# Kernel optimization log

Hardware: AMD Instinct MI355X
Metric: run time of the kernel (lower is better)

The kernel has to match this reference:

```python
import jax, jax.numpy as jnp
import numpy as np
import math

B = 8; SEQ = 1000; C_IN = 32; D = 512; H = 8; DK = 64; DV = 64
DFF = 2048; NL = 4; ARY = 4; INNER = 5


def get_mask_np(seq_size, ary, inner):
    # full k-ary tree sizes (padded) and effective sizes per scale
    full = 1
    while full < seq_size:
        full *= ary
    all_size = [full]; effe = [seq_size]
    while all_size[-1] > 1:
        all_size.append(all_size[-1] // ary)
        effe.append(math.ceil(effe[-1] / ary))
    n = sum(all_size)
    allow = np.zeros((n, n), dtype=bool)
    w = inner // 2
    starts = np.concatenate([[0], np.cumsum(all_size)]).astype(int)
    # intra-scale local window
    for l, sz in enumerate(all_size):
        s = starts[l]
        for i in range(sz):
            lo = max(i - w, 0); hi = min(i + w + 1, sz)
            allow[s + i, s + lo:s + hi] = True
    # inter-scale parent<->children links
    for l in range(1, len(all_size)):
        s = starts[l]; ps = starts[l - 1]
        for i in range(all_size[l]):
            lo = ps + i * ary; hi = ps + (i + 1) * ary
            allow[s + i, lo:hi] = True
            allow[lo:hi, s + i] = True
    return allow, all_size, effe

ALLOW_NP, ALL_SIZE, EFFE_SIZE = get_mask_np(SEQ, ARY, INNER)
NTOT = sum(ALL_SIZE)   # 1365
DEPTH = len(ALL_SIZE)  # 6
OFFS = np.concatenate([[0], np.cumsum(ALL_SIZE)]).astype(int)


def sinusoid_pe(length, d):
    pos = np.arange(length)[:, None].astype(np.float64)
    i = np.arange(d)[None, :]
    ang = pos / np.power(10000.0, (2 * (i // 2)) / d)
    pe = np.zeros((length, d), np.float32)
    pe[:, 0::2] = np.sin(ang[:, 0::2]); pe[:, 1::2] = np.cos(ang[:, 1::2])
    return pe

PE_NP = sinusoid_pe(SEQ, D)


def layer_norm(x, s, b, eps=1e-5):
    m = x.mean(-1, keepdims=True)
    v = ((x - m) ** 2).mean(-1, keepdims=True)
    return (x - m) * jax.lax.rsqrt(v + eps) * s + b


def setup_inputs() -> dict:
    key = jax.random.key(0)
    ks = jax.random.split(key, 10)
    p = lambda k, shape, sc=0.02: jax.random.normal(k, shape, jnp.float32) * sc
    return {
        "x": jax.random.normal(ks[0], (B, SEQ, C_IN), jnp.float32),
        "conv_w": p(ks[1], (D, C_IN, 3), 0.05),
        "norm_s": jnp.ones((D,), jnp.float32), "norm_b": jnp.zeros((D,), jnp.float32),
        "wq": p(ks[2], (NL, D, H * DK)), "wk": p(ks[3], (NL, D, H * DK)),
        "wv": p(ks[4], (NL, D, H * DV)), "wo": p(ks[5], (NL, H * DV, D)),
        "ln1_s": jnp.ones((NL, D), jnp.float32), "ln1_b": jnp.zeros((NL, D), jnp.float32),
        "w1": p(ks[6], (NL, D, DFF)), "b1": jnp.zeros((NL, DFF), jnp.float32),
        "w2": p(ks[7], (NL, DFF, D)), "b2": jnp.zeros((NL, D), jnp.float32),
        "ln2_s": jnp.ones((NL, D), jnp.float32), "ln2_b": jnp.zeros((NL, D), jnp.float32),
    }


def reference(x, conv_w, norm_s, norm_b, wq, wk, wv, wo, ln1_s, ln1_b,
              w1, b1, w2, b2, ln2_s, ln2_b):
    allow = jnp.asarray(ALLOW_NP)        # [N,N] True = attend
    pe = jnp.asarray(PE_NP)              # [S,D]
    # --- DataEmbedding: conv1d(k=3, circular pad, no bias) + sinusoid PE ---
    xt = jnp.concatenate([x[:, -1:], x, x[:, :1]], axis=1)       # (B,S+2,C)
    emb = jax.lax.conv_general_dilated(
        xt, conv_w, (1,), 'VALID', dimension_numbers=('NWC', 'OIW', 'NWC'))
    emb = emb + pe[None]                                          # (B,S,D)
    # pad sequence to full-tree leaf count
    emb = jnp.pad(emb, ((0, 0), (0, ALL_SIZE[0] - SEQ), (0, 0)))  # (B,L0,D)
    # --- MaxPooling_Construct: pool by ary per level, concat, LayerNorm ---
    parts = [emb]
    cur = emb
    for lvl in range(DEPTH - 1):
        L = cur.shape[1]
        cur = cur.reshape(B, L // ARY, ARY, D).max(axis=2)
        parts.append(cur)
    seq = jnp.concatenate(parts, axis=1)                          # (B,N,D)
    seq = layer_norm(seq, norm_s, norm_b)
    # --- masked MHA encoder layers (post-norm) ---
    scale = 1.0 / math.sqrt(DK)
    neg = jnp.float32(-1e9)
    for l in range(NL):
        q = (seq @ wq[l]).reshape(B, NTOT, H, DK)
        k = (seq @ wk[l]).reshape(B, NTOT, H, DK)
        v = (seq @ wv[l]).reshape(B, NTOT, H, DV)
        scores = jnp.einsum('bnhd,bmhd->bhnm', q, k) * scale
        scores = jnp.where(allow[None, None], scores, neg)
        attn = jax.nn.softmax(scores, axis=-1)
        ctx = jnp.einsum('bhnm,bmhd->bnhd', attn, v).reshape(B, NTOT, H * DV)
        seq = layer_norm(seq + ctx @ wo[l], ln1_s[l], ln1_b[l])
        ff = jax.nn.gelu(seq @ w1[l] + b1[l], approximate=False) @ w2[l] + b2[l]
        seq = layer_norm(seq + ff, ln2_s[l], ln2_b[l])
    # --- keep only the effective (unpadded) prefix of each scale ---
    out = jnp.concatenate(
        [seq[:, OFFS[i]:OFFS[i] + EFFE_SIZE[i]] for i in range(DEPTH)], axis=1)
    return out  # (B, sum(effe)=1334, D)
```

## Files before the change

kernel.cpp:

```cpp
#include <hip/hip_runtime.h>
#include <cstdint>
#include <math.h>

#define DEV __device__ __forceinline__

static constexpr int BQ = 8, SEQN = 1000, CIN = 32, NH = 8;
static constexpr int NLAY = 4;
static constexpr int NTOT_C = 1365;
static constexpr int M_REAL = BQ * NTOT_C;
static constexpr int M_PAD  = 11008;

DEV float bf2f(unsigned short u){ return __uint_as_float(((unsigned)u) << 16); }
DEV unsigned short f2bf(float f){
  unsigned u = __float_as_uint(f);
  u += 0x7fffu + ((u >> 16) & 1u);
  return (unsigned short)(u >> 16);
}

typedef __bf16 bf16x8 __attribute__((ext_vector_type(8)));
typedef float  f32x4  __attribute__((ext_vector_type(4)));
typedef unsigned short u16x8 __attribute__((ext_vector_type(8)));

#define GLD_LDS16(gp, lp) __builtin_amdgcn_global_load_lds( \
    (const __attribute__((address_space(1))) void*)(gp), \
    (__attribute__((address_space(3))) void*)(lp), 16, 0, 0)

template<int N> DEV void waitcnt_vm(){
  asm volatile("s_waitcnt vmcnt(%0)" :: "i"(N) : "memory");
}
DEV void waitcnt_lgkm0(){ asm volatile("s_waitcnt lgkmcnt(0)" ::: "memory"); }
DEV void cfence(){ asm volatile("" ::: "memory"); }

DEV float gelu_f(float x){
  float z = 0.7978845608028654f * (x + 0.044715f * x * x * x);
  z = fminf(fmaxf(z, -10.f), 10.f);
  float e = __expf(2.f * z);
  float th = (e - 1.f) / (e + 1.f);
  return 0.5f * x * (1.f + th);
}

__global__ __launch_bounds__(256) void pe_kernel(float* __restrict__ pe)
{
  int idx = blockIdx.x * 256 + threadIdx.x;
  int d = idx & 511, s = idx >> 9;
  if (s >= SEQN) return;
  float e2 = (float)(d & ~1);
  float freq = exp2f(e2 * (-13.287712379549449f / 512.0f));
  float ang = (float)s * freq;
  pe[idx] = (d & 1) ? cosf(ang) : sinf(ang);
}

__global__ __launch_bounds__(256) void conv_kernel(const float* __restrict__ x,
    const float* __restrict__ w, const float* __restrict__ pe, float* __restrict__ seqf)
{
  __shared__ float ws_w[128 * 97];
  __shared__ __align__(16) float xs[66][32];
  int b = blockIdx.z, s0 = blockIdx.y * 64, d0 = blockIdx.x * 128;
  int tid = threadIdx.x;
  for (int i = tid; i < 128 * 96; i += 256){
    int r = i / 96, c = i - r * 96;
    ws_w[r * 97 + c] = w[(size_t)(d0 + r) * 96 + c];
  }
  for (int i = tid; i < 66 * 32; i += 256){
    int r = i >> 5, c = i & 31;
    int ss = s0 + r - 1;
    ss = (ss < 0) ? (ss + SEQN) : (ss >= SEQN ? ss - SEQN : ss);
    xs[r][c] = x[((size_t)b * SEQN + ss) * CIN + c];
  }
  __syncthreads();
  int dl = tid & 127, sh = tid >> 7;
  float wr[96];
  #pragma unroll
  for (int i = 0; i < 96; i++) wr[i] = ws_w[dl * 97 + i];
  int d = d0 + dl;
  for (int si = 0; si < 32; si++){
    int sl = sh * 32 + si;
    int s = s0 + sl;
    float acc = 0.f;
    #pragma unroll
    for (int kk = 0; kk < 3; kk++){
      const float* xr = xs[sl + kk];
      #pragma unroll
      for (int c = 0; c < 32; c++) acc += xr[c] * wr[c * 3 + kk];
    }
    float outv = (s < SEQN) ? acc + pe[(size_t)s * 512 + d] : 0.f;
    seqf[((size_t)b * NTOT_C + s) * 512 + d] = outv;
  }
}

__global__ __launch_bounds__(256) void pool_kernel(float* __restrict__ seqf,
    int inOff, int outOff, int outSz)
{
  int e = blockIdx.x * 256 + threadIdx.x;
  int d = e & 511;
  int r = e >> 9;
  int i = r % outSz;
  int b = r / outSz;
  const float* src = seqf + ((size_t)b * NTOT_C + inOff + 4 * i) * 512 + d;
  float m = fmaxf(fmaxf(src[0], src[512]), fmaxf(src[1024], src[1536]));
  seqf[((size_t)b * NTOT_C + outOff + i) * 512 + d] = m;
}

__global__ __launch_bounds__(256) void ln4_kernel(const float* __restrict__ xin,
    float* __restrict__ outf, unsigned short* __restrict__ outb,
    const float* __restrict__ sg, const float* __restrict__ bg, int M)
{
  int row = blockIdx.x * 4 + (threadIdx.x >> 6);
  int lane = threadIdx.x & 63;
  size_t base = (size_t)row * 512 + lane * 8;
  if (row >= M){
    f32x4 z4 = {0.f, 0.f, 0.f, 0.f};
    *reinterpret_cast<f32x4*>(outf + base) = z4;
    *reinterpret_cast<f32x4*>(outf + base + 4) = z4;
    u16x8 z8 = {0, 0, 0, 0, 0, 0, 0, 0};
    *reinterpret_cast<u16x8*>(outb + base) = z8;
    return;
  }
  f32x4 v0 = *reinterpret_cast<const f32x4*>(xin + base);
  f32x4 v1 = *reinterpret_cast<const f32x4*>(xin + base + 4);
  float sall = v0[0] + v0[1] + v0[2] + v0[3] + v1[0] + v1[1] + v1[2] + v1[3];
  #pragma unroll
  for (int o = 32; o; o >>= 1) sall += __shfl_xor(sall, o, 64);
  float mean = sall * (1.f / 512.f);
  float d[8];
  #pragma unroll
  for (int e = 0; e < 4; e++){ d[e] = v0[e] - mean; d[4 + e] = v1[e] - mean; }
  float sq = 0.f;
  #pragma unroll
  for (int e = 0; e < 8; e++) sq += d[e] * d[e];
  #pragma unroll
  for (int o = 32; o; o >>= 1) sq += __shfl_xor(sq, o, 64);
  float rstd = 1.f / sqrtf(sq * (1.f / 512.f) + 1e-5f);
  f32x4 s0 = *reinterpret_cast<const f32x4*>(sg + lane * 8);
  f32x4 s1 = *reinterpret_cast<const f32x4*>(sg + lane * 8 + 4);
  f32x4 g0 = *reinterpret_cast<const f32x4*>(bg + lane * 8);
  f32x4 g1 = *reinterpret_cast<const f32x4*>(bg + lane * 8 + 4);
  f32x4 y0, y1; u16x8 yb;
  #pragma unroll
  for (int e = 0; e < 4; e++){
    y0[e] = d[e] * rstd * s0[e] + g0[e];
    y1[e] = d[4 + e] * rstd * s1[e] + g1[e];
    yb[e] = f2bf(y0[e]); yb[4 + e] = f2bf(y1[e]);
  }
  *reinterpret_cast<f32x4*>(outf + base) = y0;
  *reinterpret_cast<f32x4*>(outf + base + 4) = y1;
  *reinterpret_cast<u16x8*>(outb + base) = yb;
}

template<bool WRITEF>
__global__ __launch_bounds__(256) void lnres4_kernel(const unsigned short* __restrict__ cin,
    float* __restrict__ outf, unsigned short* __restrict__ seqb,
    const float* __restrict__ sg, const float* __restrict__ bg, int M)
{
  int row = blockIdx.x * 4 + (threadIdx.x >> 6);
  int lane = threadIdx.x & 63;
  size_t base = (size_t)row * 512 + lane * 8;
  if (row >= M){
    u16x8 z8 = {0, 0, 0, 0, 0, 0, 0, 0};
    *reinterpret_cast<u16x8*>(seqb + base) = z8;
    if (WRITEF){
      f32x4 z4 = {0.f, 0.f, 0.f, 0.f};
      *reinterpret_cast<f32x4*>(outf + base) = z4;
      *reinterpret_cast<f32x4*>(outf + base + 4) = z4;
    }
    return;
  }
  u16x8 cv = *reinterpret_cast<const u16x8*>(cin + base);
  u16x8 rv = *reinterpret_cast<const u16x8*>(seqb + base);
  float v[8];
  #pragma unroll
  for (int e = 0; e < 8; e++) v[e] = bf2f(cv[e]) + bf2f(rv[e]);
  float sall = 0.f;
  #pragma unroll
  for (int e = 0; e < 8; e++) sall += v[e];
  #pragma unroll
  for (int o = 32; o; o >>= 1) sall += __shfl_xor(sall, o, 64);
  float mean = sall * (1.f / 512.f);
  float sq = 0.f;
  #pragma unroll
  for (int e = 0; e < 8; e++){ v[e] -= mean; sq += v[e] * v[e]; }
  #pragma unroll
  for (int o = 32; o; o >>= 1) sq += __shfl_xor(sq, o, 64);
  float rstd = 1.f / sqrtf(sq * (1.f / 512.f) + 1e-5f);
  f32x4 s0 = *reinterpret_cast<const f32x4*>(sg + lane * 8);
  f32x4 s1 = *reinterpret_cast<const f32x4*>(sg + lane * 8 + 4);
  f32x4 g0 = *reinterpret_cast<const f32x4*>(bg + lane * 8);
  f32x4 g1 = *reinterpret_cast<const f32x4*>(bg + lane * 8 + 4);
  u16x8 yb; f32x4 y0, y1;
  #pragma unroll
  for (int e = 0; e < 4; e++){
    y0[e] = v[e] * rstd * s0[e] + g0[e];
    y1[e] = v[4 + e] * rstd * s1[e] + g1[e];
    yb[e] = f2bf(y0[e]); yb[4 + e] = f2bf(y1[e]);
  }
  *reinterpret_cast<u16x8*>(seqb + base) = yb;
  if (WRITEF){
    *reinterpret_cast<f32x4*>(outf + base) = y0;
    *reinterpret_cast<f32x4*>(outf + base + 4) = y1;
  }
}

__global__ __launch_bounds__(256) void wconv_all(
    const float* __restrict__ wq, const float* __restrict__ wk,
    const float* __restrict__ wv, const float* __restrict__ wo,
    const float* __restrict__ w1, const float* __restrict__ w2,
    unsigned short* __restrict__ qkvT, unsigned short* __restrict__ woT,
    unsigned short* __restrict__ w1T, unsigned short* __restrict__ w2T)
{
  __shared__ float tile[32][33];
  int bid = blockIdx.x;
  const float* wl; unsigned short* wtl; int N, K, n0, k0;
  if (bid < 4096){
    int part = bid >> 10, t = bid & 1023;
    int l = t >> 8, t2 = t & 255;
    k0 = (t2 >> 4) * 32; n0 = (t2 & 15) * 32;
    N = 512; K = 512;
    const float* s = (part == 0) ? wq : (part == 1) ? wk : (part == 2) ? wv : wo;
    wl = s + (size_t)l * 512 * 512;
    wtl = (part < 3) ? (qkvT + (size_t)l * 1536 * 512 + (size_t)part * 512 * 512)
                     : (woT + (size_t)l * 512 * 512);
  } else if (bid < 8192){
    int t = bid - 4096, l = t >> 10, t2 = t & 1023;
    k0 = (t2 >> 6) * 32; n0 = (t2 & 63) * 32;
    N = 2048; K = 512;
    wl = w1 + (size_t)l * 512 * 2048;
    wtl = w1T + (size_t)l * 2048 * 512;
  } else {
    int t = bid - 8192, l = t >> 10, t2 = t & 1023;
    k0 = (t2 >> 4) * 32; n0 = (t2 & 15) * 32;
    N = 512; K = 2048;
    wl = w2 + (size_t)l * 2048 * 512;
    wtl = w2T + (size_t)l * 512 * 2048;
  }
  int c = threadIdx.x & 31, r8 = threadIdx.x >> 5;
  #pragma unroll
  for (int p = 0; p < 4; p++){ int r = r8 + p * 8; tile[r][c] = wl[(size_t)(k0 + r) * N + n0 + c]; }
  __syncthreads();
  #pragma unroll
  for (int p = 0; p < 4; p++){ int r = r8 + p * 8; wtl[(size_t)(n0 + r) * K + k0 + c] = f2bf(tile[c][r]); }
}

template<int EPI, int BM, int BN>
__global__ __launch_bounds__(256) void gemm2_kernel(
    const unsigned short* __restrict__ A, const unsigned short* __restrict__ Wt,
    unsigned short* __restrict__ Cb, const float* __restrict__ bias, int N, int K)
{
  constexpr int MF = BM / 32, NF = BN / 32;
  constexpr int LA = BM / 32, LB = BN / 32;
  __shared__ __align__(16) unsigned short Abuf[2][BM * 64];
  __shared__ __align__(16) unsigned short Bbuf[2][BN * 64];
  const int tid = threadIdx.x;
  const int wid = tid >> 6, lane = tid & 63;
  const int wm2 = wid >> 1, wn2 = wid & 1;
  const int r16 = lane & 15, g = lane >> 4;
  const int m0 = blockIdx.y * BM, n0 = blockIdx.x * BN;

  const int row0 = tid >> 3;
  const int scol = ((tid & 7) ^ (row0 & 7)) * 8;
  const unsigned short* gAs = A  + (size_t)(m0 + row0) * K + scol;
  const unsigned short* gBs = Wt + (size_t)(n0 + row0) * K + scol;

  const int swz0 = ((0 + g) ^ (r16 & 7)) * 8;
  const int swz1 = ((4 + g) ^ (r16 & 7)) * 8;
  const int arow = (wm2 * (BM / 2) + r16) * 64;
  const int brow = (wn2 * (BN / 2) + r16) * 64;

  const int nt = K >> 6;
  f32x4 acc[MF][NF] = {};

  auto STAGE_A = [&](int buf, int kt){
    #pragma unroll
    for (int q = 0; q < LA; q++)
      GLD_LDS16(gAs + kt * 64 + (size_t)q * 32 * K, &Abuf[buf][q * 2048 + tid * 8]);
  };
  auto STAGE_B = [&](int buf, int kt){
    #pragma unroll
    for (int q = 0; q < LB; q++)
      GLD_LDS16(gBs + kt * 64 + (size_t)q * 32 * K, &Bbuf[buf][q * 2048 + tid * 8]);
  };

  cfence();
  STAGE_A(0, 0); STAGE_B(0, 0);
  if (nt > 1){ STAGE_A(1, 1); waitcnt_vm<LA>(); }
  else        { waitcnt_vm<0>(); }
  __builtin_amdgcn_s_barrier();
  cfence();

  for (int t = 0; t < nt; t++){
    const int d = t & 1;
    const unsigned short* Ab = Abuf[d];
    const unsigned short* Bb = Bbuf[d];

    bf16x8 a0[MF], b0[NF];
    #pragma unroll
    for (int m = 0; m < MF; m++) a0[m] = *reinterpret_cast<const bf16x8*>(&Ab[arow + m * 1024 + swz0]);
    #pragma unroll
    for (int n = 0; n < NF; n++) b0[n] = *reinterpret_cast<const bf16x8*>(&Bb[brow + n * 1024 + swz0]);
    if (t + 1 < nt){ cfence(); STAGE_B(d ^ 1, t + 1); cfence(); }
    __builtin_amdgcn_s_setprio(1);
    #pragma unroll
    for (int m = 0; m < MF; m++)
      #pragma unroll
      for (int n = 0; n < NF; n++)
        acc[m][n] = __builtin_amdgcn_mfma_f32_16x16x32_bf16(a0[m], b0[n], acc[m][n], 0, 0, 0);
    __builtin_amdgcn_s_setprio(0);

    bf16x8 a1[MF], b1v[NF];
    #pragma unroll
    for (int m = 0; m < MF; m++) a1[m] = *reinterpret_cast<const bf16x8*>(&Ab[arow + m * 1024 + swz1]);
    #pragma unroll
    for (int n = 0; n < NF; n++) b1v[n] = *reinterpret_cast<const bf16x8*>(&Bb[brow + n * 1024 + swz1]);
    waitcnt_lgkm0();
    __builtin_amdgcn_s_barrier();
    cfence();
    if (t + 2 < nt){ STAGE_A(d, t + 2); cfence(); }
    __builtin_amdgcn_s_setprio(1);
    #pragma unroll
    for (int m = 0; m < MF; m++)
      #pragma unroll
      for (int n = 0; n < NF; n++)
        acc[m][n] = __builtin_amdgcn_mfma_f32_16x16x32_bf16(a1[m], b1v[n], acc[m][n], 0, 0, 0);
    __builtin_amdgcn_s_setprio(0);

    if (t + 1 < nt){
      if (t + 2 < nt) waitcnt_vm<LA>();
      else            waitcnt_vm<0>();
      __builtin_amdgcn_s_barrier();
      cfence();
    }
  }

  const int colBase = n0 + wn2 * (BN / 2) + r16;
  #pragma unroll
  for (int m = 0; m < MF; m++){
    int row = m0 + wm2 * (BM / 2) + m * 16 + g * 4;
    #pragma unroll
    for (int n = 0; n < NF; n++){
      int col = colBase + n * 16;
      float bsv = (EPI >= 2) ? bias[col] : 0.f;
      #pragma unroll
      for (int j = 0; j < 4; j++){
        float v = acc[m][n][j];
        if (EPI >= 2) v += bsv;
        if (EPI == 2) v = gelu_f(v);
        Cb[(size_t)(row + j) * N + col] = f2bf(v);
      }
    }
  }
}

__global__ __launch_bounds__(256) void attn_kernel(
    const unsigned short* __restrict__ qkv, unsigned short* __restrict__ ctx)
{
  int wid = blockIdx.x * 4 + (threadIdx.x >> 6);
  int lane = threadIdx.x & 63;
  int n = wid % NTOT_C;
  int b = wid / NTOT_C;

  int i, sz, of, cb, par;
  if (n < 1024){ i = n;        sz = 1024; of = 0;    cb = -1;            par = 1024 + (i >> 2); }
  else if (n < 1280){ i = n - 1024; sz = 256; of = 1024; cb = 0    + 4 * i; par = 1280 + (i >> 2); }
  else if (n < 1344){ i = n - 1280; sz = 64;  of = 1280; cb = 1024 + 4 * i; par = 1344 + (i >> 2); }
  else if (n < 1360){ i = n - 1344; sz = 16;  of = 1344; cb = 1280 + 4 * i; par = 1360 + (i >> 2); }
  else if (n < 1364){ i = n - 1360; sz = 4;   of = 1360; cb = 1344 + 4 * i; par = 1364; }
  else { i = 0; sz = 1; of = 1364; cb = 1360; par = -1; }

  int nb[10];
  #pragma unroll
  for (int s5 = 0; s5 < 5; s5++){ int pos = i - 2 + s5; nb[s5] = (pos >= 0 && pos < sz) ? of + pos : -1; }
  #pragma unroll
  for (int r = 0; r < 4; r++) nb[5 + r] = (cb >= 0) ? cb + r : -1;
  nb[9] = par;

  const unsigned short* rows = qkv + ((size_t)b * NTOT_C) * 1536;

  u16x8 qv = *reinterpret_cast<const u16x8*>(rows + (size_t)n * 1536 + lane * 8);
  float qf[8];
  #pragma unroll
  for (int e = 0; e < 8; e++) qf[e] = bf2f(qv[e]);

  float sc[10];
  #pragma unroll
  for (int j = 0; j < 10; j++){
    int id = nb[j] >= 0 ? nb[j] : n;
    u16x8 kv = *reinterpret_cast<const u16x8*>(rows + (size_t)id * 1536 + 512 + lane * 8);
    float p = 0.f;
    #pragma unroll
    for (int e = 0; e < 8; e++) p += qf[e] * bf2f(kv[e]);
    p += __shfl_xor(p, 1, 64);
    p += __shfl_xor(p, 2, 64);
    p += __shfl_xor(p, 4, 64);
    sc[j] = (nb[j] >= 0) ? p * 0.125f : -1e30f;
  }
  float mx = sc[0];
  #pragma unroll
  for (int j = 1; j < 10; j++) mx = fmaxf(mx, sc[j]);
  float den = 0.f;
  float wj[10];
  #pragma unroll
  for (int j = 0; j < 10; j++){
    wj[j] = (nb[j] >= 0) ? expf(sc[j] - mx) : 0.f;
    den += wj[j];
  }
  float rden = 1.f / den;
  float accv[8] = {};
  #pragma unroll
  for (int j = 0; j < 10; j++){
    int id = nb[j] >= 0 ? nb[j] : n;
    u16x8 vv = *reinterpret_cast<const u16x8*>(rows + (size_t)id * 1536 + 1024 + lane * 8);
    float w = wj[j];
    #pragma unroll
    for (int e = 0; e < 8; e++) accv[e] += w * bf2f(vv[e]);
  }
  u16x8 ov;
  #pragma unroll
  for (int e = 0; e < 8; e++) ov[e] = f2bf(accv[e] * rden);
  *reinterpret_cast<u16x8*>(ctx + ((size_t)b * NTOT_C + n) * 512 + lane * 8) = ov;
}

__global__ __launch_bounds__(256) void gather_kernel(const float* __restrict__ seqf,
    float* __restrict__ out)
{
  int e = blockIdx.x * 256 + threadIdx.x;
  int d = e & 511;
  int r = e >> 9;
  int j = r % 1334;
  int b = r / 1334;
  int src;
  if      (j < 1000) src = j;
  else if (j < 1250) src = j + 24;
  else if (j < 1313) src = j + 30;
  else if (j < 1333) src = j + 31;
  else               src = 1364;
  out[e] = seqf[((size_t)b * NTOT_C + src) * 512 + d];
}

extern "C" void kernel_launch(void* const* d_in, const int* in_sizes, int n_in,
                              void* d_out, int out_size, void* d_ws, size_t ws_size,
                              hipStream_t stream)
{
  const float* x      = (const float*)d_in[0];
  const float* conv_w = (const float*)d_in[1];
  const float* norm_s = (const float*)d_in[2];
  const float* norm_b = (const float*)d_in[3];
  const float* wq     = (const float*)d_in[4];
  const float* wk     = (const float*)d_in[5];
  const float* wv     = (const float*)d_in[6];
  const float* wo     = (const float*)d_in[7];
  const float* ln1_s  = (const float*)d_in[8];
  const float* ln1_b  = (const float*)d_in[9];
  const float* w1     = (const float*)d_in[10];
  const float* b1     = (const float*)d_in[11];
  const float* w2     = (const float*)d_in[12];
  const float* b2     = (const float*)d_in[13];
  const float* ln2_s  = (const float*)d_in[14];
  const float* ln2_b  = (const float*)d_in[15];
  float* out = (float*)d_out;

  char* ws = (char*)d_ws;
  size_t off = 0;
  auto alloc = [&](size_t bytes) -> char* {
    char* p = ws + off; off += (bytes + 255) & ~(size_t)255; return p;
  };
  unsigned short* qkvT = (unsigned short*)alloc((size_t)NLAY * 1536 * 512 * 2);
  unsigned short* woT  = (unsigned short*)alloc((size_t)NLAY * 512 * 512 * 2);
  unsigned short* w1T  = (unsigned short*)alloc((size_t)NLAY * 2048 * 512 * 2);
  unsigned short* w2T  = (unsigned short*)alloc((size_t)NLAY * 512 * 2048 * 2);
  float*          seqf = (float*)alloc((size_t)M_PAD * 512 * 4);
  unsigned short* seqb = (unsigned short*)alloc((size_t)M_PAD * 512 * 2);
  float*          buff = (float*)alloc((size_t)M_PAD * 512 * 4);
  unsigned short* qkvb = (unsigned short*)alloc((size_t)M_PAD * 1536 * 2);
  unsigned short* ctxb = (unsigned short*)alloc((size_t)M_PAD * 512 * 2);
  unsigned short* ffn1 = qkvb;
  float*          pe   = buff;
  unsigned short* delta = (unsigned short*)buff;

  wconv_all<<<12288, 256, 0, stream>>>(wq, wk, wv, wo, w1, w2, qkvT, woT, w1T, w2T);

  pe_kernel<<<(SEQN * 512) / 256, 256, 0, stream>>>(pe);
  conv_kernel<<<dim3(4,16,BQ), 256, 0, stream>>>(x, conv_w, pe, seqf);
  const int psz[6]  = {1024, 256, 64, 16, 4, 1};
  const int poff[6] = {0, 1024, 1280, 1344, 1360, 1364};
  for (int l = 0; l < 5; l++)
    pool_kernel<<<(BQ * psz[l+1] * 512) / 256, 256, 0, stream>>>(seqf, poff[l], poff[l+1], psz[l+1]);
  ln4_kernel<<<M_PAD / 4, 256, 0, stream>>>(seqf, seqf, seqb, norm_s, norm_b, M_REAL);

  for (int l = 0; l < NLAY; l++){
    gemm2_kernel<1,128,128><<<dim3(12,86),256,0,stream>>>(seqb, qkvT + (size_t)l*1536*512, qkvb, nullptr, 1536, 512);
    attn_kernel<<<(BQ * NTOT_C + 3) / 4, 256, 0, stream>>>(qkvb, ctxb);
    gemm2_kernel<1,64,128><<<dim3(4,172),256,0,stream>>>(ctxb, woT + (size_t)l*512*512, delta, nullptr, 512, 512);
    lnres4_kernel<false><<<M_PAD / 4,256,0,stream>>>(delta, seqf, seqb, ln1_s + l*512, ln1_b + l*512, M_REAL);
    gemm2_kernel<2,128,128><<<dim3(16,86),256,0,stream>>>(seqb, w1T + (size_t)l*2048*512, ffn1, b1 + l*2048, 2048, 512);
    gemm2_kernel<4,64,128><<<dim3(4,172),256,0,stream>>>(ffn1, w2T + (size_t)l*512*2048, delta, b2 + l*512, 512, 2048);
    if (l < NLAY - 1)
      lnres4_kernel<false><<<M_PAD / 4,256,0,stream>>>(delta, seqf, seqb, ln2_s + l*512, ln2_b + l*512, M_REAL);
    else
      lnres4_kernel<true><<<M_PAD / 4,256,0,stream>>>(delta, seqf, seqb, ln2_s + l*512, ln2_b + l*512, M_REAL);
  }

  gather_kernel<<<(BQ * 1334 * 512) / 256, 256, 0, stream>>>(seqf, out);
}
```

Before: 748.2 us.

## Replace double-buffered GEMM pipeline with single-buffer K=32 tiles

Replaces the double-buffered, software-pipelined GEMM (K tile 64, async LDS staging overlapped with MFMA, explicit waitcnt and priority hints) with a simple single-buffer kernel using K tile 32 and __syncthreads around each load/compute step. LDS use drops by about four times, which could raise occupancy, but global-to-LDS loads no longer overlap MFMA work and each block now hits twice as many barriers. Latency hiding then depends on other resident blocks.

```diff
diff --git a/kernel.cpp b/kernel.cpp
--- a/kernel.cpp
+++ b/kernel.cpp
@@ -24,12 +24,6 @@
 #define GLD_LDS16(gp, lp) __builtin_amdgcn_global_load_lds( \
     (const __attribute__((address_space(1))) void*)(gp), \
     (__attribute__((address_space(3))) void*)(lp), 16, 0, 0)
-
-template<int N> DEV void waitcnt_vm(){
-  asm volatile("s_waitcnt vmcnt(%0)" :: "i"(N) : "memory");
-}
-DEV void waitcnt_lgkm0(){ asm volatile("s_waitcnt lgkmcnt(0)" ::: "memory"); }
-DEV void cfence(){ asm volatile("" ::: "memory"); }
 
 DEV float gelu_f(float x){
   float z = 0.7978845608028654f * (x + 0.044715f * x * x * x);
@@ -241,93 +235,49 @@
 }
 
 template<int EPI, int BM, int BN>
-__global__ __launch_bounds__(256) void gemm2_kernel(
+__global__ __launch_bounds__(256) void gemm3_kernel(
     const unsigned short* __restrict__ A, const unsigned short* __restrict__ Wt,
     unsigned short* __restrict__ Cb, const float* __restrict__ bias, int N, int K)
 {
   constexpr int MF = BM / 32, NF = BN / 32;
-  constexpr int LA = BM / 32, LB = BN / 32;
-  __shared__ __align__(16) unsigned short Abuf[2][BM * 64];
-  __shared__ __align__(16) unsigned short Bbuf[2][BN * 64];
+  __shared__ __align__(16) unsigned short As[BM * 32];
+  __shared__ __align__(16) unsigned short Bs[BN * 32];
   const int tid = threadIdx.x;
   const int wid = tid >> 6, lane = tid & 63;
   const int wm2 = wid >> 1, wn2 = wid & 1;
   const int r16 = lane & 15, g = lane >> 4;
   const int m0 = blockIdx.y * BM, n0 = blockIdx.x * BN;
 
-  const int row0 = tid >> 3;
-  const int scol = ((tid & 7) ^ (row0 & 7)) * 8;
+  const int row0 = tid >> 2;
+  const int scol = ((tid & 3) ^ ((row0 >> 1) & 3)) * 8;
   const unsigned short* gAs = A  + (size_t)(m0 + row0) * K + scol;
   const unsigned short* gBs = Wt + (size_t)(n0 + row0) * K + scol;
 
-  const int swz0 = ((0 + g) ^ (r16 & 7)) * 8;
-  const int swz1 = ((4 + g) ^ (r16 & 7)) * 8;
-  const int arow = (wm2 * (BM / 2) + r16) * 64;
-  const int brow = (wn2 * (BN / 2) + r16) * 64;
-
-  const int nt = K >> 6;
+  const int swz = (g ^ ((r16 >> 1) & 3)) * 8;
+  const int nt = K >> 5;
   f32x4 acc[MF][NF] = {};
 
-  auto STAGE_A = [&](int buf, int kt){
-    #pragma unroll
-    for (int q = 0; q < LA; q++)
-      GLD_LDS16(gAs + kt * 64 + (size_t)q * 32 * K, &Abuf[buf][q * 2048 + tid * 8]);
-  };
-  auto STAGE_B = [&](int buf, int kt){
-    #pragma unroll
-    for (int q = 0; q < LB; q++)
-      GLD_LDS16(gBs + kt * 64 + (size_t)q * 32 * K, &Bbuf[buf][q * 2048 + tid * 8]);
-  };
-
-  cfence();
-  STAGE_A(0, 0); STAGE_B(0, 0);
-  if (nt > 1){ STAGE_A(1, 1); waitcnt_vm<LA>(); }
-  else        { waitcnt_vm<0>(); }
-  __builtin_amdgcn_s_barrier();
-  cfence();
-
   for (int t = 0; t < nt; t++){
-    const int d = t & 1;
-    const unsigned short* Ab = Abuf[d];
-    const unsigned short* Bb = Bbuf[d];
-
-    bf16x8 a0[MF], b0[NF];
-    #pragma unroll
-    for (int m = 0; m < MF; m++) a0[m] = *reinterpret_cast<const bf16x8*>(&Ab[arow + m * 1024 + swz0]);
-    #pragma unroll
-    for (int n = 0; n < NF; n++) b0[n] = *reinterpret_cast<const bf16x8*>(&Bb[brow + n * 1024 + swz0]);
-    if (t + 1 < nt){ cfence(); STAGE_B(d ^ 1, t + 1); cfence(); }
-    __builtin_amdgcn_s_setprio(1);
+    #pragma unroll
+    for (int q = 0; q < BM / 64; q++)
+      GLD_LDS16(gAs + t * 32 + (size_t)q * 64 * K, &As[q * 2048 + tid * 8]);
+    #pragma unroll
+    for (int q = 0; q < BN / 64; q++)
+      GLD_LDS16(gBs + t * 32 + (size_t)q * 64 * K, &Bs[q * 2048 + tid * 8]);
+    __syncthreads();
+    bf16x8 av[MF], bv[NF];
+    #pragma unroll
+    for (int m = 0; m < MF; m++)
+      av[m] = *reinterpret_cast<const bf16x8*>(&As[(wm2 * (BM / 2) + m * 16 + r16) * 32 + swz]);
+    #pragma unroll
+    for (int n = 0; n < NF; n++)
+      bv[n] = *reinterpret_cast<const bf16x8*>(&Bs[(wn2 * (BN / 2) + n * 16 + r16) * 32 + swz]);
     #pragma unroll
     for (int m = 0; m < MF; m++)
       #pragma unroll
       for (int n = 0; n < NF; n++)
-        acc[m][n] = __builtin_amdgcn_mfma_f32_16x16x32_bf16(a0[m], b0[n], acc[m][n], 0, 0, 0);
-    __builtin_amdgcn_s_setprio(0);
-
-    bf16x8 a1[MF], b1v[NF];
-    #pragma unroll
-    for (int m = 0; m < MF; m++) a1[m] = *reinterpret_cast<const bf16x8*>(&Ab[arow + m * 1024 + swz1]);
-    #pragma unroll
-    for (int n = 0; n < NF; n++) b1v[n] = *reinterpret_cast<const bf16x8*>(&Bb[brow + n * 1024 + swz1]);
-    waitcnt_lgkm0();
-    __builtin_amdgcn_s_barrier();
-    cfence();
-    if (t + 2 < nt){ STAGE_A(d, t + 2); cfence(); }
-    __builtin_amdgcn_s_setprio(1);
-    #pragma unroll
-    for (int m = 0; m < MF; m++)
-      #pragma unroll
-      for (int n = 0; n < NF; n++)
-        acc[m][n] = __builtin_amdgcn_mfma_f32_16x16x32_bf16(a1[m], b1v[n], acc[m][n], 0, 0, 0);
-    __builtin_amdgcn_s_setprio(0);
-
-    if (t + 1 < nt){
-      if (t + 2 < nt) waitcnt_vm<LA>();
-      else            waitcnt_vm<0>();
-      __builtin_amdgcn_s_barrier();
-      cfence();
-    }
+        acc[m][n] = __builtin_amdgcn_mfma_f32_16x16x32_bf16(av[m], bv[n], acc[m][n], 0, 0, 0);
+    if (t + 1 < nt) __syncthreads();
   }
 
   const int colBase = n0 + wn2 * (BN / 2) + r16;
@@ -486,12 +436,12 @@
   ln4_kernel<<<M_PAD / 4, 256, 0, stream>>>(seqf, seqf, seqb, norm_s, norm_b, M_REAL);
 
   for (int l = 0; l < NLAY; l++){
-    gemm2_kernel<1,128,128><<<dim3(12,86),256,0,stream>>>(seqb, qkvT + (size_t)l*1536*512, qkvb, nullptr, 1536, 512);
+    gemm3_kernel<1,128,128><<<dim3(12,86),256,0,stream>>>(seqb, qkvT + (size_t)l*1536*512, qkvb, nullptr, 1536, 512);
     attn_kernel<<<(BQ * NTOT_C + 3) / 4, 256, 0, stream>>>(qkvb, ctxb);
-    gemm2_kernel<1,64,128><<<dim3(4,172),256,0,stream>>>(ctxb, woT + (size_t)l*512*512, delta, nullptr, 512, 512);
+    gemm3_kernel<1,64,128><<<dim3(4,172),256,0,stream>>>(ctxb, woT + (size_t)l*512*512, delta, nullptr, 512, 512);
     lnres4_kernel<false><<<M_PAD / 4,256,0,stream>>>(delta, seqf, seqb, ln1_s + l*512, ln1_b + l*512, M_REAL);
-    gemm2_kernel<2,128,128><<<dim3(16,86),256,0,stream>>>(seqb, w1T + (size_t)l*2048*512, ffn1, b1 + l*2048, 2048, 512);
-    gemm2_kernel<4,64,128><<<dim3(4,172),256,0,stream>>>(ffn1, w2T + (size_t)l*512*2048, delta, b2 + l*512, 512, 2048);
+    gemm3_kernel<2,128,128><<<dim3(16,86),256,0,stream>>>(seqb, w1T + (size_t)l*2048*512, ffn1, b1 + l*2048, 2048, 512);
+    gemm3_kernel<4,64,128><<<dim3(4,172),256,0,stream>>>(ffn1, w2T + (size_t)l*512*2048, delta, b2 + l*512, 512, 2048);
     if (l < NLAY - 1)
       lnres4_kernel<false><<<M_PAD / 4,256,0,stream>>>(delta, seqf, seqb, ln2_s + l*512, ln2_b + l*512, M_REAL);
     else
```

Result: slower. 808.4 us (+8.1%).
